# Kernel optimization log

Hardware: AMD Instinct MI355X
Metric: run time of the kernel (lower is better)

The kernel has to match this reference:

```python
import jax, jax.numpy as jnp
import numpy as np

B, T, E = 16, 2048, 768   # batch, frames, encoder dim
C, D = 504, 256           # num_classes, final_dim
EPS = 1e-8                # torch cosine_similarity eps
LOGIT_TEMP = 0.1


def _normalize(v):
    n = jnp.maximum(jnp.linalg.norm(v, axis=-1, keepdims=True), EPS)
    return v / n


def _compute_logits(proj_x, target, emb):
    # proj_x: [N, D], target: [N] int, emb: [C, D]
    pxn = _normalize(proj_x)
    embn = _normalize(emb)
    pos = jnp.take(embn, target, axis=0)            # [N, D]
    pos_logit = jnp.sum(pxn * pos, axis=-1)          # [N]
    neg_logits = pxn @ embn.T                        # [N, C] fused normalize+matmul
    # neg_is_pos: class row identical to the positive row (distinct random rows => class == label)
    neg_is_pos = jnp.arange(emb.shape[0])[None, :] == target[:, None]
    neg_logits = jnp.where(neg_is_pos, -jnp.inf, neg_logits)
    logits = jnp.concatenate([pos_logit[:, None], neg_logits], axis=1)  # [N, 1+C]
    return logits / LOGIT_TEMP


def setup_inputs() -> dict:
    key = jax.random.key(0)
    k1, k2, k3, k4, k5 = jax.random.split(key, 5)
    x = jax.random.normal(k1, (B, T, E), dtype=jnp.float32)
    label = jax.random.randint(k2, (B, T), 0, C)
    mask_m = jnp.ones((B, T), dtype=bool)
    mask_u = jnp.ones((B, T), dtype=bool)
    bound = 1.0 / np.sqrt(E)
    W = jax.random.uniform(k3, (D, E), minval=-bound, maxval=bound, dtype=jnp.float32)
    b = jax.random.uniform(k4, (D,), minval=-bound, maxval=bound, dtype=jnp.float32)
    emb = jax.random.uniform(k5, (C, D), dtype=jnp.float32)  # torch.nn.init.uniform_ default [0,1)
    return {"x": x, "label": label, "mask_m": mask_m, "mask_u": mask_u,
            "W": W, "b": b, "emb": emb}


def reference(x, label, mask_m, mask_u, W, b, emb):
    proj_x = jnp.einsum('bte,de->btd', x, W) + b        # final_proj
    pf = proj_x.reshape(-1, D)
    lf = label.reshape(-1)
    idx_m = jnp.nonzero(mask_m.reshape(-1))[0]          # concrete masks -> static shapes
    idx_u = jnp.nonzero(mask_u.reshape(-1))[0]
    logit_m = _compute_logits(pf[idx_m], lf[idx_m], emb)
    logit_u = _compute_logits(pf[idx_u], lf[idx_u], emb)
    return (logit_m, logit_u)
```

## Files before the change

kernel.cpp:

```cpp
#include <hip/hip_runtime.h>
#include <hip/hip_bf16.h>
#include <math.h>

#define N_ROWS 32768
#define E_DIM  768
#define D_DIM  256
#define C_CLS  504
#define C_PAD  512
#define N_OUT  505
#define EPS    1e-8f
#define NEG_BIG (-1e30f)

typedef __attribute__((ext_vector_type(8))) __bf16 bf16x8;
typedef __attribute__((ext_vector_type(4))) float f32x4;

#define MFMA16(a, b, c) __builtin_amdgcn_mfma_f32_16x16x32_bf16((a), (b), (c), 0, 0, 0)

#define GLDS16(g, l)                                                   \
    __builtin_amdgcn_global_load_lds(                                  \
        (const __attribute__((address_space(1))) void*)(g),            \
        (__attribute__((address_space(3))) void*)(l), 16, 0, 0)

__global__ __launch_bounds__(256) void convert_w_kernel(const float* __restrict__ W,
                                                        __bf16* __restrict__ Wh) {
    const int idx = blockIdx.x * 256 + threadIdx.x;
    const float4 v = ((const float4*)W)[idx];
    union { __bf16 h[4]; uint2 u; } pk;
    pk.h[0] = (__bf16)v.x; pk.h[1] = (__bf16)v.y;
    pk.h[2] = (__bf16)v.z; pk.h[3] = (__bf16)v.w;
    ((uint2*)Wh)[idx] = pk.u;
}

__global__ __launch_bounds__(256) void convert_x_kernel(const float* __restrict__ x,
                                                        __bf16* __restrict__ xh) {
    const int idx = blockIdx.x * 256 + threadIdx.x;
    const float4 v0 = ((const float4*)x)[idx * 2];
    const float4 v1 = ((const float4*)x)[idx * 2 + 1];
    union { __bf16 h[8]; uint4 u; } pk;
    pk.h[0] = (__bf16)v0.x; pk.h[1] = (__bf16)v0.y;
    pk.h[2] = (__bf16)v0.z; pk.h[3] = (__bf16)v0.w;
    pk.h[4] = (__bf16)v1.x; pk.h[5] = (__bf16)v1.y;
    pk.h[6] = (__bf16)v1.z; pk.h[7] = (__bf16)v1.w;
    ((uint4*)xh)[idx] = pk.u;
}

__global__ __launch_bounds__(64) void embnorm_kernel(const float* __restrict__ emb,
                                                     __bf16* __restrict__ embnh) {
    const int c = blockIdx.x;
    const int lane = threadIdx.x;
    union { __bf16 h[4]; uint2 u; } pk;
    if (c < C_CLS) {
        const float4 v = ((const float4*)(emb + (size_t)c * D_DIM))[lane];
        float s = v.x * v.x + v.y * v.y + v.z * v.z + v.w * v.w;
        #pragma unroll
        for (int off = 32; off; off >>= 1) s += __shfl_xor(s, off);
        const float inv = 1.0f / fmaxf(sqrtf(s), EPS);
        pk.h[0] = (__bf16)(v.x * inv); pk.h[1] = (__bf16)(v.y * inv);
        pk.h[2] = (__bf16)(v.z * inv); pk.h[3] = (__bf16)(v.w * inv);
    } else {
        pk.h[0] = (__bf16)0.0f; pk.h[1] = (__bf16)0.0f;
        pk.h[2] = (__bf16)0.0f; pk.h[3] = (__bf16)0.0f;
    }
    ((uint2*)(embnh + (size_t)c * D_DIM))[lane] = pk.u;
}


__global__ __launch_bounds__(256) void gemm1_mfma(const __bf16* __restrict__ xh,
                                                  const __bf16* __restrict__ Wh,
                                                  const float* __restrict__ bias,
                                                  __bf16* __restrict__ projn) {
    __shared__ __bf16 As[64 * 64];
    __shared__ __bf16 Bs[256 * 64];
    __shared__ float sos[4][64];

    const int tid  = threadIdx.x;
    const int w    = tid >> 6;
    const int lane = tid & 63;
    const int l15  = lane & 15;
    const int quad = lane >> 4;
    const int row0 = blockIdx.x * 64;

    f32x4 acc[4][4] = {};

    for (int k0 = 0; k0 < E_DIM; k0 += 64) {
        #pragma unroll
        for (int c = 0; c < 2; ++c) {
            const int o   = tid * 16 + c * 4096;
            const int row = o >> 7;
            const int sc  = ((o >> 4) & 7) ^ (row & 7);
            GLDS16(xh + (size_t)(row0 + row) * E_DIM + k0 + sc * 8,
                   (char*)As + c * 4096 + (w << 10));
        }
        #pragma unroll
        for (int c = 0; c < 8; ++c) {
            const int o   = tid * 16 + c * 4096;
            const int row = o >> 7;
            const int sc  = ((o >> 4) & 7) ^ (row & 7);
            GLDS16(Wh + (size_t)row * E_DIM + k0 + sc * 8,
                   (char*)Bs + c * 4096 + (w << 10));
        }
        __syncthreads();

        #pragma unroll
        for (int kk = 0; kk < 2; ++kk) {
            const int chunk = (quad + 4 * kk) ^ (l15 & 7);
            bf16x8 af[4], bf[4];
            #pragma unroll
            for (int m = 0; m < 4; ++m)
                af[m] = *(const bf16x8*)((const char*)As +
                          (m * 16 + l15) * 128 + (chunk << 4));
            #pragma unroll
            for (int n = 0; n < 4; ++n)
                bf[n] = *(const bf16x8*)((const char*)Bs +
                          (w * 64 + n * 16 + l15) * 128 + (chunk << 4));
            #pragma unroll
            for (int m = 0; m < 4; ++m)
                #pragma unroll
                for (int n = 0; n < 4; ++n)
                    acc[m][n] = MFMA16(af[m], bf[n], acc[m][n]);
        }
        __syncthreads();
    }

    float bv[4];
    #pragma unroll
    for (int n = 0; n < 4; ++n) bv[n] = bias[w * 64 + n * 16 + l15];

    #pragma unroll
    for (int m = 0; m < 4; ++m)
        #pragma unroll
        for (int r = 0; r < 4; ++r) {
            float t = 0.0f;
            #pragma unroll
            for (int n = 0; n < 4; ++n) {
                const float v = acc[m][n][r] + bv[n];
                acc[m][n][r] = v;
                t += v * v;
            }
            t += __shfl_xor(t, 1);
            t += __shfl_xor(t, 2);
            t += __shfl_xor(t, 4);
            t += __shfl_xor(t, 8);
            if (l15 == 0) sos[w][m * 16 + quad * 4 + r] = t;
        }
    __syncthreads();
    #pragma unroll
    for (int m = 0; m < 4; ++m)
        #pragma unroll
        for (int r = 0; r < 4; ++r) {
            const int R = m * 16 + quad * 4 + r;
            const float tot = sos[0][R] + sos[1][R] + sos[2][R] + sos[3][R];
            const float inv = 1.0f / fmaxf(sqrtf(tot), EPS);
            __bf16* op = projn + (size_t)(row0 + R) * D_DIM + w * 64 + l15;
            #pragma unroll
            for (int n = 0; n < 4; ++n)
                op[n * 16] = (__bf16)(acc[m][n][r] * inv);
        }
}

__global__ __launch_bounds__(256) void gemm2_mfma(const __bf16* __restrict__ projn,
                                                  const __bf16* __restrict__ embnh,
                                                  const int* __restrict__ label,
                                                  float* __restrict__ outm,
                                                  float* __restrict__ outu) {
    __shared__ char smem[40960];
    __shared__ int labs[64];
    __bf16* As = (__bf16*)smem;
    __bf16* Bs = (__bf16*)(smem + 8192);
    float (*obuf)[260] = (float (*)[260])smem;
    float* posv = (float*)(smem + 33280);

    const int tid  = threadIdx.x;
    const int w    = tid >> 6;
    const int lane = tid & 63;
    const int l15  = lane & 15;
    const int quad = lane >> 4;
    const int row0 = blockIdx.x * 64;
    const int c0   = blockIdx.y * 256;

    if (tid < 64) labs[tid] = label[row0 + tid];

    f32x4 acc[4][4] = {};

    for (int k0 = 0; k0 < D_DIM; k0 += 64) {
        #pragma unroll
        for (int c = 0; c < 2; ++c) {
            const int o   = tid * 16 + c * 4096;
            const int row = o >> 7;
            const int sc  = ((o >> 4) & 7) ^ (row & 7);
            GLDS16(projn + (size_t)(row0 + row) * D_DIM + k0 + sc * 8,
                   (char*)As + c * 4096 + (w << 10));
        }
        #pragma unroll
        for (int c = 0; c < 8; ++c) {
            const int o   = tid * 16 + c * 4096;
            const int row = o >> 7;
            const int sc  = ((o >> 4) & 7) ^ (row & 7);
            GLDS16(embnh + (size_t)(c0 + row) * D_DIM + k0 + sc * 8,
                   (char*)Bs + c * 4096 + (w << 10));
        }
        __syncthreads();

        #pragma unroll
        for (int kk = 0; kk < 2; ++kk) {
            const int chunk = (quad + 4 * kk) ^ (l15 & 7);
            bf16x8 af[4], bf[4];
            #pragma unroll
            for (int m = 0; m < 4; ++m)
                af[m] = *(const bf16x8*)((const char*)As +
                          (m * 16 + l15) * 128 + (chunk << 4));
            #pragma unroll
            for (int n = 0; n < 4; ++n)
                bf[n] = *(const bf16x8*)((const char*)Bs +
                          (w * 64 + n * 16 + l15) * 128 + (chunk << 4));
            #pragma unroll
            for (int m = 0; m < 4; ++m)
                #pragma unroll
                for (int n = 0; n < 4; ++n)
                    acc[m][n] = MFMA16(af[m], bf[n], acc[m][n]);
        }
        __syncthreads();
    }

    #pragma unroll
    for (int g = 0; g < 2; ++g) {
        #pragma unroll
        for (int mi = 0; mi < 2; ++mi) {
            const int m = g * 2 + mi;
            #pragma unroll
            for (int r = 0; r < 4; ++r) {
                const int lrow = mi * 16 + quad * 4 + r;
                const int lab  = labs[g * 32 + lrow];
                #pragma unroll
                for (int n = 0; n < 4; ++n) {
                    const int cl = w * 64 + n * 16 + l15;
                    const int c  = c0 + cl;
                    const float val = acc[m][n][r] * 10.0f;
                    const bool pos = (c == lab);
                    obuf[lrow][cl] = pos ? NEG_BIG : val;
                    if (pos) posv[lrow] = val;
                }
            }
        }
        __syncthreads();
        {
            const int c = c0 + tid;
            if (c < C_CLS) {
                #pragma unroll
                for (int r = 0; r < 32; ++r) {
                    const size_t base = (size_t)(row0 + g * 32 + r) * N_OUT;
                    const float v = obuf[r][tid];
                    outm[base + 1 + c] = v;
                    outu[base + 1 + c] = v;
                }
            }
        }
        if (tid < 32) {
            const int gr = g * 32 + tid;
            const int lab = labs[gr];
            if (lab >= c0 && lab < c0 + 256) {
                const size_t base = (size_t)(row0 + gr) * N_OUT;
                const float v = posv[tid];
                outm[base] = v;
                outu[base] = v;
            }
        }
        __syncthreads();
    }
}

extern "C" void kernel_launch(void* const* d_in, const int* in_sizes, int n_in,
                              void* d_out, int out_size, void* d_ws, size_t ws_size,
                              hipStream_t stream) {
    const float* x     = (const float*)d_in[0];
    const int*   label = (const int*)d_in[1];
    const float* W     = (const float*)d_in[4];
    const float* b     = (const float*)d_in[5];
    const float* emb   = (const float*)d_in[6];
    float* out = (float*)d_out;

    char* ws = (char*)d_ws;
    __bf16* Wh    = (__bf16*)ws;
    __bf16* embnh = (__bf16*)(ws + 393216);
    __bf16* projn = (__bf16*)(ws + 393216 + 262144);
    __bf16* xh    = (__bf16*)(ws + 393216 + 262144 + 16777216);

    convert_w_kernel<<<192, 256, 0, stream>>>(W, Wh);
    embnorm_kernel<<<C_PAD, 64, 0, stream>>>(emb, embnh);
    convert_x_kernel<<<12288, 256, 0, stream>>>(x, xh);
    gemm1_mfma<<<N_ROWS / 64, 256, 0, stream>>>(xh, Wh, b, projn);
    gemm2_mfma<<<dim3(N_ROWS / 64, 2), 256, 0, stream>>>(
        projn, embnh, label, out, out + (size_t)N_ROWS * N_OUT);
}
```

Baseline: 286.0 us.

## Fuse fp32-to-bf16 conversion of x into the projection GEMM A-tile load

Removes the separate convert_x kernel and its bf16 copy of x. The projection GEMM now reads fp32 x directly into registers, converts it to bf16 and writes it swizzled into LDS. The next k-tile of x is prefetched into registers while the current one is processed. This drops a full write and re-read of the 48MB-equivalent intermediate and one launch, at the cost of more registers and register-staged loads in place of direct global-to-LDS loads.

```diff
diff --git a/kernel.cpp b/kernel.cpp
--- a/kernel.cpp
+++ b/kernel.cpp
@@ -29,19 +29,6 @@
     pk.h[0] = (__bf16)v.x; pk.h[1] = (__bf16)v.y;
     pk.h[2] = (__bf16)v.z; pk.h[3] = (__bf16)v.w;
     ((uint2*)Wh)[idx] = pk.u;
-}
-
-__global__ __launch_bounds__(256) void convert_x_kernel(const float* __restrict__ x,
-                                                        __bf16* __restrict__ xh) {
-    const int idx = blockIdx.x * 256 + threadIdx.x;
-    const float4 v0 = ((const float4*)x)[idx * 2];
-    const float4 v1 = ((const float4*)x)[idx * 2 + 1];
-    union { __bf16 h[8]; uint4 u; } pk;
-    pk.h[0] = (__bf16)v0.x; pk.h[1] = (__bf16)v0.y;
-    pk.h[2] = (__bf16)v0.z; pk.h[3] = (__bf16)v0.w;
-    pk.h[4] = (__bf16)v1.x; pk.h[5] = (__bf16)v1.y;
-    pk.h[6] = (__bf16)v1.z; pk.h[7] = (__bf16)v1.w;
-    ((uint4*)xh)[idx] = pk.u;
 }
 
 __global__ __launch_bounds__(64) void embnorm_kernel(const float* __restrict__ emb,
@@ -65,7 +52,7 @@
 }
 
 
-__global__ __launch_bounds__(256) void gemm1_mfma(const __bf16* __restrict__ xh,
+__global__ __launch_bounds__(256) void gemm1_mfma(const float* __restrict__ x,
                                                   const __bf16* __restrict__ Wh,
                                                   const float* __restrict__ bias,
                                                   __bf16* __restrict__ projn) {
@@ -80,17 +67,21 @@
     const int quad = lane >> 4;
     const int row0 = blockIdx.x * 64;
 
+    const int ar  = tid >> 2;
+    const int aks = (tid & 3) * 16;
+    const float* axp = x + (size_t)(row0 + ar) * E_DIM + aks;
+    const int ac0 = aks >> 3;
+    char* awp0 = (char*)As + ar * 128 + ((ac0       ^ (ar & 7)) << 4);
+    char* awp1 = (char*)As + ar * 128 + (((ac0 + 1) ^ (ar & 7)) << 4);
+
     f32x4 acc[4][4] = {};
 
+    float4 aq0 = *(const float4*)(axp);
+    float4 aq1 = *(const float4*)(axp + 4);
+    float4 aq2 = *(const float4*)(axp + 8);
+    float4 aq3 = *(const float4*)(axp + 12);
+
     for (int k0 = 0; k0 < E_DIM; k0 += 64) {
-        #pragma unroll
-        for (int c = 0; c < 2; ++c) {
-            const int o   = tid * 16 + c * 4096;
-            const int row = o >> 7;
-            const int sc  = ((o >> 4) & 7) ^ (row & 7);
-            GLDS16(xh + (size_t)(row0 + row) * E_DIM + k0 + sc * 8,
-                   (char*)As + c * 4096 + (w << 10));
-        }
         #pragma unroll
         for (int c = 0; c < 8; ++c) {
             const int o   = tid * 16 + c * 4096;
@@ -99,6 +90,26 @@
             GLDS16(Wh + (size_t)row * E_DIM + k0 + sc * 8,
                    (char*)Bs + c * 4096 + (w << 10));
         }
+        const int kn = k0 + 64;
+        float4 nq0, nq1, nq2, nq3;
+        if (kn < E_DIM) {
+            nq0 = *(const float4*)(axp + kn);
+            nq1 = *(const float4*)(axp + kn + 4);
+            nq2 = *(const float4*)(axp + kn + 8);
+            nq3 = *(const float4*)(axp + kn + 12);
+        }
+        union { __bf16 h[16]; uint4 q[2]; } pk;
+        pk.h[0]  = (__bf16)aq0.x; pk.h[1]  = (__bf16)aq0.y;
+        pk.h[2]  = (__bf16)aq0.z; pk.h[3]  = (__bf16)aq0.w;
+        pk.h[4]  = (__bf16)aq1.x; pk.h[5]  = (__bf16)aq1.y;
+        pk.h[6]  = (__bf16)aq1.z; pk.h[7]  = (__bf16)aq1.w;
+        pk.h[8]  = (__bf16)aq2.x; pk.h[9]  = (__bf16)aq2.y;
+        pk.h[10] = (__bf16)aq2.z; pk.h[11] = (__bf16)aq2.w;
+        pk.h[12] = (__bf16)aq3.x; pk.h[13] = (__bf16)aq3.y;
+        pk.h[14] = (__bf16)aq3.z; pk.h[15] = (__bf16)aq3.w;
+        *(uint4*)awp0 = pk.q[0];
+        *(uint4*)awp1 = pk.q[1];
+
         __syncthreads();
 
         #pragma unroll
@@ -119,6 +130,7 @@
                 for (int n = 0; n < 4; ++n)
                     acc[m][n] = MFMA16(af[m], bf[n], acc[m][n]);
         }
+        aq0 = nq0; aq1 = nq1; aq2 = nq2; aq3 = nq3;
         __syncthreads();
     }
 
@@ -283,12 +295,10 @@
     __bf16* Wh    = (__bf16*)ws;
     __bf16* embnh = (__bf16*)(ws + 393216);
     __bf16* projn = (__bf16*)(ws + 393216 + 262144);
-    __bf16* xh    = (__bf16*)(ws + 393216 + 262144 + 16777216);
 
     convert_w_kernel<<<192, 256, 0, stream>>>(W, Wh);
     embnorm_kernel<<<C_PAD, 64, 0, stream>>>(emb, embnh);
-    convert_x_kernel<<<12288, 256, 0, stream>>>(x, xh);
-    gemm1_mfma<<<N_ROWS / 64, 256, 0, stream>>>(xh, Wh, b, projn);
+    gemm1_mfma<<<N_ROWS / 64, 256, 0, stream>>>(x, Wh, b, projn);
     gemm2_mfma<<<dim3(N_ROWS / 64, 2), 256, 0, stream>>>(
         projn, embnh, label, out, out + (size_t)N_ROWS * N_OUT);
 }
```

New measurement: 270.2 us. 1.06x faster.

## Fuse x conversion into gemm1 and double-buffer LDS in both GEMMs

Applied to the files above, without the earlier changes.

Drops the separate fp32-to-bf16 conversion kernel for x. gemm1 now loads fp32 x directly into registers, converts it, and stores it into a double-buffered LDS tile with K=32 stages, with loads prefetched two steps ahead. gemm2 is also switched to double-buffered K=32 stages so the async global-to-LDS copies overlap the MFMA work. This removes a full write and re-read of the bf16 copy of x. In exchange there are more barriers per K step and higher register pressure from the prefetched fp32 values.

```diff
diff --git a/kernel.cpp b/kernel.cpp
--- a/kernel.cpp
+++ b/kernel.cpp
@@ -31,19 +31,6 @@
     ((uint2*)Wh)[idx] = pk.u;
 }
 
-__global__ __launch_bounds__(256) void convert_x_kernel(const float* __restrict__ x,
-                                                        __bf16* __restrict__ xh) {
-    const int idx = blockIdx.x * 256 + threadIdx.x;
-    const float4 v0 = ((const float4*)x)[idx * 2];
-    const float4 v1 = ((const float4*)x)[idx * 2 + 1];
-    union { __bf16 h[8]; uint4 u; } pk;
-    pk.h[0] = (__bf16)v0.x; pk.h[1] = (__bf16)v0.y;
-    pk.h[2] = (__bf16)v0.z; pk.h[3] = (__bf16)v0.w;
-    pk.h[4] = (__bf16)v1.x; pk.h[5] = (__bf16)v1.y;
-    pk.h[6] = (__bf16)v1.z; pk.h[7] = (__bf16)v1.w;
-    ((uint4*)xh)[idx] = pk.u;
-}
-
 __global__ __launch_bounds__(64) void embnorm_kernel(const float* __restrict__ emb,
                                                      __bf16* __restrict__ embnh) {
     const int c = blockIdx.x;
@@ -65,12 +52,12 @@
 }
 
 
-__global__ __launch_bounds__(256) void gemm1_mfma(const __bf16* __restrict__ xh,
+__global__ __launch_bounds__(256) void gemm1_mfma(const float* __restrict__ x,
                                                   const __bf16* __restrict__ Wh,
                                                   const float* __restrict__ bias,
                                                   __bf16* __restrict__ projn) {
-    __shared__ __bf16 As[64 * 64];
-    __shared__ __bf16 Bs[256 * 64];
+    __shared__ __bf16 As[2][64 * 32];
+    __shared__ __bf16 Bs[2][256 * 32];
     __shared__ float sos[4][64];
 
     const int tid  = threadIdx.x;
@@ -80,47 +67,78 @@
     const int quad = lane >> 4;
     const int row0 = blockIdx.x * 64;
 
+    const int ar   = tid >> 2;
+    const int ach  = tid & 3;
+    const float* axp = x + (size_t)(row0 + ar) * E_DIM + ach * 8;
+    const int aoff = ar * 64 + ((ach ^ ((ar >> 1) & 3)) << 4);
+
+    #define G1_STAGE_B(buf, kt)                                              \
+        _Pragma("unroll")                                                    \
+        for (int c = 0; c < 4; ++c) {                                        \
+            const int row = c * 64 + (tid >> 2);                             \
+            const int sc  = (tid & 3) ^ ((row >> 1) & 3);                    \
+            GLDS16(Wh + (size_t)row * E_DIM + (kt) * 32 + sc * 8,            \
+                   (char*)Bs[buf] + c * 4096 + (w << 10));                   \
+        }
+
+    float4 aq0 = *(const float4*)(axp);
+    float4 aq1 = *(const float4*)(axp + 4);
+    G1_STAGE_B(0, 0);
+    {
+        union { __bf16 h[8]; uint4 q; } pk;
+        pk.h[0] = (__bf16)aq0.x; pk.h[1] = (__bf16)aq0.y;
+        pk.h[2] = (__bf16)aq0.z; pk.h[3] = (__bf16)aq0.w;
+        pk.h[4] = (__bf16)aq1.x; pk.h[5] = (__bf16)aq1.y;
+        pk.h[6] = (__bf16)aq1.z; pk.h[7] = (__bf16)aq1.w;
+        *(uint4*)((char*)As[0] + aoff) = pk.q;
+    }
+    aq0 = *(const float4*)(axp + 32);
+    aq1 = *(const float4*)(axp + 36);
+    __syncthreads();
+
     f32x4 acc[4][4] = {};
 
-    for (int k0 = 0; k0 < E_DIM; k0 += 64) {
-        #pragma unroll
-        for (int c = 0; c < 2; ++c) {
-            const int o   = tid * 16 + c * 4096;
-            const int row = o >> 7;
-            const int sc  = ((o >> 4) & 7) ^ (row & 7);
-            GLDS16(xh + (size_t)(row0 + row) * E_DIM + k0 + sc * 8,
-                   (char*)As + c * 4096 + (w << 10));
-        }
-        #pragma unroll
-        for (int c = 0; c < 8; ++c) {
-            const int o   = tid * 16 + c * 4096;
-            const int row = o >> 7;
-            const int sc  = ((o >> 4) & 7) ^ (row & 7);
-            GLDS16(Wh + (size_t)row * E_DIM + k0 + sc * 8,
-                   (char*)Bs + c * 4096 + (w << 10));
-        }
+    #pragma unroll
+    for (int t = 0; t < 24; ++t) {
+        const int cur = t & 1;
+        const int nxt = cur ^ 1;
+        float4 nq0, nq1;
+        if (t + 2 < 24) {
+            nq0 = *(const float4*)(axp + (t + 2) * 32);
+            nq1 = *(const float4*)(axp + (t + 2) * 32 + 4);
+        }
+        if (t + 1 < 24) {
+            G1_STAGE_B(nxt, t + 1);
+            union { __bf16 h[8]; uint4 q; } pk;
+            pk.h[0] = (__bf16)aq0.x; pk.h[1] = (__bf16)aq0.y;
+            pk.h[2] = (__bf16)aq0.z; pk.h[3] = (__bf16)aq0.w;
+            pk.h[4] = (__bf16)aq1.x; pk.h[5] = (__bf16)aq1.y;
+            pk.h[6] = (__bf16)aq1.z; pk.h[7] = (__bf16)aq1.w;
+            *(uint4*)((char*)As[nxt] + aoff) = pk.q;
+        }
+        bf16x8 af[4], bf[4];
+        #pragma unroll
+        for (int m = 0; m < 4; ++m) {
+            const int row = m * 16 + l15;
+            af[m] = *(const bf16x8*)((const char*)As[cur] + row * 64 +
+                      ((quad ^ ((row >> 1) & 3)) << 4));
+        }
+        #pragma unroll
+        for (int n = 0; n < 4; ++n) {
+            const int row = w * 64 + n * 16 + l15;
+            bf[n] = *(const bf16x8*)((const char*)Bs[cur] + row * 64 +
+                      ((quad ^ ((row >> 1) & 3)) << 4));
+        }
+        #pragma unroll
+        for (int m = 0; m < 4; ++m)
+            #pragma unroll
+            for (int n = 0; n < 4; ++n)
+                acc[m][n] = MFMA16(af[m], bf[n], acc[m][n]);
+
         __syncthreads();
-
-        #pragma unroll
-        for (int kk = 0; kk < 2; ++kk) {
-            const int chunk = (quad + 4 * kk) ^ (l15 & 7);
-            bf16x8 af[4], bf[4];
-            #pragma unroll
-            for (int m = 0; m < 4; ++m)
-                af[m] = *(const bf16x8*)((const char*)As +
-                          (m * 16 + l15) * 128 + (chunk << 4));
-            #pragma unroll
-            for (int n = 0; n < 4; ++n)
-                bf[n] = *(const bf16x8*)((const char*)Bs +
-                          (w * 64 + n * 16 + l15) * 128 + (chunk << 4));
-            #pragma unroll
-            for (int m = 0; m < 4; ++m)
-                #pragma unroll
-                for (int n = 0; n < 4; ++n)
-                    acc[m][n] = MFMA16(af[m], bf[n], acc[m][n]);
-        }
-        __syncthreads();
-    }
+        if (t + 2 < 24) { aq0 = nq0; aq1 = nq1; }
+    }
+    #undef G1_STAGE_B
 
     float bv[4];
     #pragma unroll
@@ -165,8 +183,6 @@
                                                   float* __restrict__ outu) {
     __shared__ char smem[40960];
     __shared__ int labs[64];
-    __bf16* As = (__bf16*)smem;
-    __bf16* Bs = (__bf16*)(smem + 8192);
     float (*obuf)[260] = (float (*)[260])smem;
     float* posv = (float*)(smem + 33280);
 
@@ -180,47 +196,57 @@
 
     if (tid < 64) labs[tid] = label[row0 + tid];
 
+    #define G2_AS(buf) (smem + (buf) * 4096)
+    #define G2_BS(buf) (smem + 8192 + (buf) * 16384)
+    #define G2_STAGE(buf, kt)                                                \
+        {                                                                    \
+            const int arow = tid >> 2;                                       \
+            const int asc  = (tid & 3) ^ ((arow >> 1) & 3);                  \
+            GLDS16(projn + (size_t)(row0 + arow) * D_DIM + (kt) * 32 + asc * 8, \
+                   G2_AS(buf) + (w << 10));                                  \
+            _Pragma("unroll")                                                \
+            for (int c = 0; c < 4; ++c) {                                    \
+                const int row = c * 64 + (tid >> 2);                         \
+                const int sc  = (tid & 3) ^ ((row >> 1) & 3);                \
+                GLDS16(embnh + (size_t)(c0 + row) * D_DIM + (kt) * 32 + sc * 8, \
+                       G2_BS(buf) + c * 4096 + (w << 10));                   \
+            }                                                                \
+        }
+
+    G2_STAGE(0, 0);
+    __syncthreads();
+
     f32x4 acc[4][4] = {};
 
-    for (int k0 = 0; k0 < D_DIM; k0 += 64) {
-        #pragma unroll
-        for (int c = 0; c < 2; ++c) {
-            const int o   = tid * 16 + c * 4096;
-            const int row = o >> 7;
-            const int sc  = ((o >> 4) & 7) ^ (row & 7);
-            GLDS16(projn + (size_t)(row0 + row) * D_DIM + k0 + sc * 8,
-                   (char*)As + c * 4096 + (w << 10));
-        }
-        #pragma unroll
-        for (int c = 0; c < 8; ++c) {
-            const int o   = tid * 16 + c * 4096;
-            const int row = o >> 7;
-            const int sc  = ((o >> 4) & 7) ^ (row & 7);
-            GLDS16(embnh + (size_t)(c0 + row) * D_DIM + k0 + sc * 8,
-                   (char*)Bs + c * 4096 + (w << 10));
-        }
+    #pragma unroll
+    for (int t = 0; t < 8; ++t) {
+        const int cur = t & 1;
+        if (t + 1 < 8) G2_STAGE(cur ^ 1, t + 1);
+
+        bf16x8 af[4], bf[4];
+        #pragma unroll
+        for (int m = 0; m < 4; ++m) {
+            const int row = m * 16 + l15;
+            af[m] = *(const bf16x8*)(G2_AS(cur) + row * 64 +
+                      ((quad ^ ((row >> 1) & 3)) << 4));
+        }
+        #pragma unroll
+        for (int n = 0; n < 4; ++n) {
+            const int row = w * 64 + n * 16 + l15;
+            bf[n] = *(const bf16x8*)(G2_BS(cur) + row * 64 +
+                      ((quad ^ ((row >> 1) & 3)) << 4));
+        }
+        #pragma unroll
+        for (int m = 0; m < 4; ++m)
+            #pragma unroll
+            for (int n = 0; n < 4; ++n)
+                acc[m][n] = MFMA16(af[m], bf[n], acc[m][n]);
+
         __syncthreads();
-
-        #pragma unroll
-        for (int kk = 0; kk < 2; ++kk) {
-            const int chunk = (quad + 4 * kk) ^ (l15 & 7);
-            bf16x8 af[4], bf[4];
-            #pragma unroll
-            for (int m = 0; m < 4; ++m)
-                af[m] = *(const bf16x8*)((const char*)As +
-                          (m * 16 + l15) * 128 + (chunk << 4));
-            #pragma unroll
-            for (int n = 0; n < 4; ++n)
-                bf[n] = *(const bf16x8*)((const char*)Bs +
-                          (w * 64 + n * 16 + l15) * 128 + (chunk << 4));
-            #pragma unroll
-            for (int m = 0; m < 4; ++m)
-                #pragma unroll
-                for (int n = 0; n < 4; ++n)
-                    acc[m][n] = MFMA16(af[m], bf[n], acc[m][n]);
-        }
-        __syncthreads();
-    }
+    }
+    #undef G2_STAGE
+    #undef G2_AS
+    #undef G2_BS
 
     #pragma unroll
     for (int g = 0; g < 2; ++g) {
@@ -283,12 +309,10 @@
     __bf16* Wh    = (__bf16*)ws;
     __bf16* embnh = (__bf16*)(ws + 393216);
     __bf16* projn = (__bf16*)(ws + 393216 + 262144);
-    __bf16* xh    = (__bf16*)(ws + 393216 + 262144 + 16777216);
 
     convert_w_kernel<<<192, 256, 0, stream>>>(W, Wh);
     embnorm_kernel<<<C_PAD, 64, 0, stream>>>(emb, embnh);
-    convert_x_kernel<<<12288, 256, 0, stream>>>(x, xh);
-    gemm1_mfma<<<N_ROWS / 64, 256, 0, stream>>>(xh, Wh, b, projn);
+    gemm1_mfma<<<N_ROWS / 64, 256, 0, stream>>>(x, Wh, b, projn);
     gemm2_mfma<<<dim3(N_ROWS / 64, 2), 256, 0, stream>>>(
         projn, embnh, label, out, out + (size_t)N_ROWS * N_OUT);
 }
```

After: 277.5 us. -3.0%, faster.
